# Kernel optimization log

Hardware: AMD Instinct MI355X
Metric: run time of the kernel (lower is better)

The kernel has to match this reference:

```python
import jax, jax.numpy as jnp
import numpy as np

B, N, D, H, L, R = 2, 2048, 1024, 16, 3, 2
HID = int(D * 2.67)
NASH_ITERS, SINK_ITERS = 3, 10
EPS = 1e-6


def _rmsnorm(x, w):
    return x * w * jax.lax.rsqrt(jnp.mean(x * x, axis=-1, keepdims=True) + EPS)


def _sinkhorn(logits):
    # Sinkhorn-Knopp projection of exp(logits) to a doubly-stochastic matrix
    M = jnp.exp(logits)
    for _ in range(SINK_ITERS):
        M = M / jnp.sum(M, axis=1, keepdims=True)
        M = M / jnp.sum(M, axis=0, keepdims=True)
    return M


def _swiglu(x, wg, wu, wd):
    return (jax.nn.silu(x @ wg) * (x @ wu)) @ wd


def _attention(xl, wq, wk, Wv):
    # causal multi-head attention at one scale; V projection (Wv) is shared across scales
    b, n, d = xl.shape
    dh = d // H
    q = (xl @ wq).reshape(b, n, H, dh)
    k = (xl @ wk).reshape(b, n, H, dh)
    v = (xl @ Wv).reshape(b, n, H, dh)
    scores = jnp.einsum('bqhd,bkhd->bhqk', q, k) / jnp.asarray(float(np.sqrt(dh)), xl.dtype)
    mask = jnp.tril(jnp.ones((n, n), bool))
    scores = jnp.where(mask, scores, jnp.asarray(-1e9, xl.dtype))
    p = jax.nn.softmax(scores, axis=-1)
    return jnp.einsum('bhqk,bkhd->bqhd', p, v).reshape(b, n, d)


def _forward(x, norm_attn_w, norm_ffn_w, W_dec, Wq, Wk, Wv, Wo, agg_logits,
             w_gate, w_up, w_down, mhc_attn_logits, mhc_ffn_logits):
    residual = x
    xn = _rmsnorm(x, norm_attn_w)
    # 1) hierarchical decomposition: avg-pool by R each level, per-scale projection
    scales = []
    cur = xn
    for l in range(L):
        scales.append(cur @ W_dec[l])
        if l < L - 1:
            b, n, d = cur.shape
            cur = cur.reshape(b, n // R, R, d).mean(axis=2)
    # 2) multiscale causal attention with shared V; upsample back to N and project
    outs = []
    for l in range(L):
        o = _attention(scales[l], Wq[l], Wk[l], Wv)
        o = jnp.repeat(o, R ** l, axis=1)  # [B, N, D]
        outs.append(o @ Wo)
    Y = jnp.stack(outs, axis=0)  # [L, B, N, D]
    # 3) Nash aggregation: best-response iterations on scale weights
    w = jax.nn.softmax(agg_logits)
    for _ in range(NASH_ITERS):
        y_bar = jnp.einsum('l,lbnd->bnd', w, Y)
        u = -jnp.mean((Y - y_bar[None]) ** 2, axis=(1, 2, 3))  # [L] payoffs
        w = jax.nn.softmax(agg_logits + u)
    attn_out = jnp.einsum('l,lbnd->bnd', w, Y)
    aux_loss = jnp.sum(w * jnp.log(w * L + 1e-9))  # KL(w || uniform)
    # 4) mHC residual mixing (attention branch): doubly-stochastic convex mix
    P = _sinkhorn(mhc_attn_logits)
    x = P[0, 0] * residual + P[0, 1] * attn_out
    # 5) SwiGLU FFN + mHC residual (FFN branch)
    residual = x
    xn = _rmsnorm(x, norm_ffn_w)
    ffn_out = _swiglu(xn, w_gate, w_up, w_down)
    P2 = _sinkhorn(mhc_ffn_logits)
    x = P2[0, 0] * residual + P2[0, 1] * ffn_out
    return x, aux_loss


def setup_inputs() -> dict:
    key = jax.random.key(0)
    ks = jax.random.split(key, 16)
    init = 0.02
    s = lambda i, shape: jax.random.normal(ks[i], shape, jnp.float32) * init
    return {
        'x': jax.random.normal(ks[0], (B, N, D), jnp.float32),
        'norm_attn_w': jnp.ones((D,), jnp.float32),
        'norm_ffn_w': jnp.ones((D,), jnp.float32),
        'W_dec': s(1, (L, D, D)),
        'Wq': s(2, (L, D, D)),
        'Wk': s(3, (L, D, D)),
        'Wv': s(4, (D, D)),
        'Wo': s(5, (D, D)),
        'agg_logits': jnp.zeros((L,), jnp.float32),
        'w_gate': s(6, (D, HID)),
        'w_up': s(7, (D, HID)),
        'w_down': s(8, (HID, D)),
        'mhc_attn_logits': jnp.zeros((2, 2), jnp.float32),
        'mhc_ffn_logits': jnp.zeros((2, 2), jnp.float32),
    }


def reference(x, norm_attn_w, norm_ffn_w, W_dec, Wq, Wk, Wv, Wo, agg_logits,
              w_gate, w_up, w_down, mhc_attn_logits, mhc_ffn_logits):
    return _forward(x, norm_attn_w, norm_ffn_w, W_dec, Wq, Wk, Wv, Wo, agg_logits,
                    w_gate, w_up, w_down, mhc_attn_logits, mhc_ffn_logits)
```

## Files before the change

kernel.cpp:

```cpp
#include <hip/hip_runtime.h>
#include <stdint.h>


#define B_   2
#define N_   2048
#define D_   1024
#define H_   16
#define DH_  64
#define HID_ 2734
#define HIDP 2816
#define CNT  (B_*N_*D_)
#define LOG2E 1.4426950408889634f

typedef unsigned short u16;
typedef __attribute__((ext_vector_type(8))) short short8;
typedef __attribute__((ext_vector_type(4))) float f32x4;
typedef __attribute__((ext_vector_type(4))) uint16_t u16x4;

__device__ __forceinline__ u16 f2bf(float f) {
  uint32_t u = __builtin_bit_cast(uint32_t, f);
  u += 0x7fffu + ((u >> 16) & 1u);
  return (u16)(u >> 16);
}
__device__ __forceinline__ float bf2f(u16 h) {
  uint32_t u = ((uint32_t)h) << 16;
  return __builtin_bit_cast(float, u);
}
__device__ __forceinline__ uint32_t pkbf(float a, float b) {
  return (uint32_t)f2bf(a) | ((uint32_t)f2bf(b) << 16);
}
__device__ __forceinline__ void gload_lds16(const void* g, void* l) {
  __builtin_amdgcn_global_load_lds(
      (const __attribute__((address_space(1))) uint32_t*)g,
      (__attribute__((address_space(3))) uint32_t*)l, 16, 0, 0);
}

__global__ __launch_bounds__(256) void wprep_k(const float* __restrict__ Wdec, const float* __restrict__ Wq,
                                               const float* __restrict__ Wk, const float* __restrict__ Wv,
                                               const float* __restrict__ Wo, const float* __restrict__ Wg,
                                               const float* __restrict__ Wu, const float* __restrict__ Wdn,
                                               u16* __restrict__ A_wp, u16* __restrict__ WdecB,
                                               u16* __restrict__ WoT, u16* __restrict__ BTgu,
                                               u16* __restrict__ WdnT, float* __restrict__ SCb) {
  const int bid = blockIdx.x;
  if (bid >= 18688) {
    if (bid == 18688 && threadIdx.x < 64) SCb[threadIdx.x] = 0.f;
    int i = (bid - 18688)*1024 + threadIdx.x*4;
    float4 v = *(const float4*)(Wdec + i);
    u16x4 o; o[0]=f2bf(v.x); o[1]=f2bf(v.y); o[2]=f2bf(v.z); o[3]=f2bf(v.w);
    *(u16x4*)(WdecB + i) = o;
    return;
  }
  const float* src; u16* dst; int K, N, KP; float scale; int imode; int bx, by;
  if (bid < 9216) {
    int j = bid >> 10, t = bid & 1023; bx = t & 31; by = t >> 5;
    int l = j / 3, which = j - l*3;
    src = which==0 ? Wq + (size_t)l*1048576 : which==1 ? Wk + (size_t)l*1048576 : Wv;
    dst = A_wp + (size_t)(l*3072 + which*1024)*1024;
    K = 1024; N = 1024; KP = 1024; scale = (which==0) ? 0.125f*LOG2E : 1.f; imode = 0;
  } else if (bid < 10240) {
    int t = bid - 9216; bx = t & 31; by = t >> 5;
    src = Wo; dst = WoT; K=1024; N=1024; KP=1024; scale=1.f; imode=0;
  } else if (bid < 13056) {
    int t = bid - 10240; bx = t % 88; by = t / 88;
    src = Wg; dst = BTgu; K=1024; N=HID_; KP=1024; scale=1.f; imode=1;
  } else if (bid < 15872) {
    int t = bid - 13056; bx = t % 88; by = t / 88;
    src = Wu; dst = BTgu; K=1024; N=HID_; KP=1024; scale=1.f; imode=2;
  } else {
    int t = bid - 15872; bx = t & 31; by = t >> 5;
    src = Wdn; dst = WdnT; K=HID_; N=1024; KP=HIDP; scale=1.f; imode=0;
  }
  __shared__ float tt[32][33];
  const int tx = threadIdx.x & 31, ty = threadIdx.x >> 5;
  const int nb = bx*32, kb = by*32;
  #pragma unroll
  for (int i = 0; i < 4; i++) {
    int k = kb + ty + i*8, n = nb + tx;
    tt[ty + i*8][tx] = (k < K && n < N) ? src[(size_t)k * N + n] * scale : 0.f;
  }
  __syncthreads();
  #pragma unroll
  for (int i = 0; i < 4; i++) {
    int n = nb + ty + i*8, k = kb + tx;
    int r;
    if (imode == 0) r = n;
    else if (imode == 1) r = ((n>>4)<<5) + (n&15);
    else r = ((n>>4)<<5) + 16 + (n&15);
    dst[(size_t)r * KP + k] = f2bf(tt[tx][ty + i*8]);
  }
}

__global__ __launch_bounds__(256) void rmsA_k(const float* __restrict__ x, const float* __restrict__ w,
                                              u16* __restrict__ xn, u16* __restrict__ xp1) {
  const int j = blockIdx.x;
  const float* xr0 = x + (size_t)(2*j) * D_;
  const float* xr1 = xr0 + D_;
  float a0[4], a1[4], wv[4];
  float ss0 = 0.f, ss1 = 0.f;
  #pragma unroll
  for (int i = 0; i < 4; i++) {
    int c = threadIdx.x + i*256;
    a0[i] = xr0[c]; a1[i] = xr1[c]; wv[i] = w[c];
    ss0 += a0[i]*a0[i]; ss1 += a1[i]*a1[i];
  }
  #pragma unroll
  for (int o = 1; o < 64; o <<= 1) { ss0 += __shfl_xor(ss0, o); ss1 += __shfl_xor(ss1, o); }
  __shared__ float r0[4], r1[4];
  if ((threadIdx.x & 63) == 0) { r0[threadIdx.x >> 6] = ss0; r1[threadIdx.x >> 6] = ss1; }
  __syncthreads();
  float sc0 = rsqrtf((r0[0]+r0[1]+r0[2]+r0[3]) * (1.f/D_) + 1e-6f);
  float sc1 = rsqrtf((r1[0]+r1[1]+r1[2]+r1[3]) * (1.f/D_) + 1e-6f);
  #pragma unroll
  for (int i = 0; i < 4; i++) {
    int c = threadIdx.x + i*256;
    float xa = a0[i]*wv[i]*sc0, xb = a1[i]*wv[i]*sc1;
    xn[(size_t)(2*j)*D_ + c]     = f2bf(xa);
    xn[(size_t)(2*j)*D_ + D_ + c] = f2bf(xb);
    xp1[(size_t)j*D_ + c] = f2bf(0.5f*(xa + xb));
  }
}

__global__ __launch_bounds__(256) void pool_k(const u16* __restrict__ in, u16* __restrict__ out, int lg) {
  const int No = 1 << lg;
  const int total4 = B_ * No * 256;
  for (int i = blockIdx.x*256 + threadIdx.x; i < total4; i += gridDim.x*256) {
    int d4 = i & 255; int j = (i >> 8) & (No - 1); int b = i >> (8 + lg);
    size_t src = ((size_t)(b*2*No + 2*j) << 10) + d4*4;
    u16x4 a = *(const u16x4*)(in + src);
    u16x4 c = *(const u16x4*)(in + src + 1024);
    u16x4 o;
    #pragma unroll
    for (int t = 0; t < 4; t++) o[t] = f2bf(0.5f * (bf2f(a[t]) + bf2f(c[t])));
    *(u16x4*)(out + (size_t)i*4) = o;
  }
}

template<int MT, int MODE>
__global__ __launch_bounds__(256) void gemm_t(const u16* __restrict__ A, const u16* __restrict__ BT,
                                              void* __restrict__ Cv, const float* __restrict__ X1,
                                              const float* __restrict__ SCp,
                                              int N, int K, int t1, int t2, unsigned int bt_stride) {
  __shared__ __align__(16) u16 As[MT*32*32];
  __shared__ __align__(16) u16 Bs[128*32];
  const int tid = threadIdx.x;
  const int lane = tid & 63, wid = tid >> 6;
  const int quad = lane >> 4, c16 = lane & 15;
  const int y = blockIdx.y;
  const int m0 = y * (MT*32), n0 = blockIdx.x * 128;
  const int wm = wid >> 1, wn = wid & 1;
  const int level = (y >= t2) ? 2 : ((y >= t1) ? 1 : 0);
  BT += (size_t)level * bt_stride;

  f32x4 acc[MT][4];
  #pragma unroll
  for (int i = 0; i < MT; i++)
    #pragma unroll
    for (int j = 0; j < 4; j++) acc[i][j] = f32x4{0.f,0.f,0.f,0.f};

  const int srow = lane >> 2;
  const int schunk = lane & 3;
  for (int k0 = 0; k0 < K; k0 += 32) {
    #pragma unroll
    for (int t = 0; t < MT/2; t++) {
      int idx = wid*(MT/2) + t;
      int row = idx*16 + srow;
      int g = (schunk ^ ((row >> 1) & 3)) * 8;
      gload_lds16(A + (size_t)(m0+row)*K + k0 + g, As + idx*512);
    }
    #pragma unroll
    for (int t = 0; t < 2; t++) {
      int idx = wid*2 + t;
      int row = idx*16 + srow;
      int g = (schunk ^ ((row >> 1) & 3)) * 8;
      gload_lds16(BT + (size_t)(n0+row)*K + k0 + g, Bs + idx*512);
    }
    __syncthreads();
    short8 af[MT], bfr[4];
    #pragma unroll
    for (int mt = 0; mt < MT; mt++) {
      int ar = wm*(MT*16) + mt*16 + c16;
      af[mt]  = *(const short8*)(As + ar*32 + (quad ^ ((ar>>1)&3))*8);
    }
    #pragma unroll
    for (int nt = 0; nt < 4; nt++) {
      int br = wn*64 + nt*16 + c16;
      bfr[nt] = *(const short8*)(Bs + br*32 + (quad ^ ((br>>1)&3))*8);
    }
    #pragma unroll
    for (int mt = 0; mt < MT; mt++)
      #pragma unroll
      for (int nt = 0; nt < 4; nt++)
        acc[mt][nt] = __builtin_amdgcn_mfma_f32_16x16x32_bf16(af[mt], bfr[nt], acc[mt][nt], 0, 0, 0);
    __syncthreads();
  }
  if (MODE == 1) {
    u16* C = (u16*)Cv;
    #pragma unroll
    for (int mt = 0; mt < MT; mt++)
      #pragma unroll
      for (int nt = 0; nt < 4; nt++)
        #pragma unroll
        for (int r = 0; r < 4; r++) {
          int row = m0 + wm*(MT*16) + mt*16 + quad*4 + r;
          int col = n0 + wn*64 + nt*16 + c16;
          C[(size_t)row * N + col] = f2bf(acc[mt][nt][r]);
        }
  } else if (MODE == 2) {
    float* C = (float*)Cv;
    const float q0 = SCp[11], q1 = SCp[12];
    #pragma unroll
    for (int mt = 0; mt < MT; mt++)
      #pragma unroll
      for (int nt = 0; nt < 4; nt++)
        #pragma unroll
        for (int r = 0; r < 4; r++) {
          int row = m0 + wm*(MT*16) + mt*16 + quad*4 + r;
          int col = n0 + wn*64 + nt*16 + c16;
          size_t o = (size_t)row * N + col;
          C[o] = q0 * X1[o] + q1 * acc[mt][nt][r];
        }
  } else {
    u16* Hc = (u16*)Cv;
    const int hbase = (n0 >> 1) + wn*32;
    #pragma unroll
    for (int mt = 0; mt < MT; mt++)
      #pragma unroll
      for (int r = 0; r < 4; r++) {
        int row = m0 + wm*(MT*16) + mt*16 + quad*4 + r;
        #pragma unroll
        for (int pr = 0; pr < 2; pr++) {
          float g = acc[mt][2*pr][r], u = acc[mt][2*pr+1][r];
          float h = g / (1.f + __expf(-g)) * u;
          Hc[(size_t)row * HIDP + hbase + pr*16 + c16] = f2bf(h);
        }
      }
  }
}

__global__ __launch_bounds__(256) void vtrans_k(const u16* __restrict__ QKV, u16* __restrict__ VTa) {
  __shared__ u16 t[32][33];
  const int bid = blockIdx.x;
  int level, tt2;
  if (bid < 4096)      { level = 0; tt2 = bid; }
  else if (bid < 6144) { level = 1; tt2 = bid - 4096; }
  else                 { level = 2; tt2 = bid - 6144; }
  const int Nl = 2048 >> level;
  const int ntiles = Nl >> 5;
  const int b = tt2 / (ntiles*32);
  const int rem = tt2 - b*(ntiles*32);
  const int c0 = (rem / ntiles) * 32;
  const int n0 = (rem - (rem / ntiles)*ntiles) * 32;
  const int rowbase = (level==0) ? 0 : (level==1) ? 4096 : 6144;
  const size_t vtoff = (level==0) ? 0 : (level==1) ? 4194304 : 6291456;
  const u16* in = QKV + (size_t)rowbase*3072 + 2048;
  u16* out = VTa + vtoff;
  const int tx = threadIdx.x & 31, ty = threadIdx.x >> 5;
  #pragma unroll
  for (int i = 0; i < 4; i++)
    t[ty + i*8][tx] = in[(size_t)(b*Nl + n0 + ty + i*8)*3072 + c0 + tx];
  __syncthreads();
  #pragma unroll
  for (int i = 0; i < 4; i++)
    out[(size_t)(b*1024 + c0 + ty + i*8)*Nl + n0 + tx] = t[tx][ty + i*8];
}

__global__ __launch_bounds__(256) void flash_k(const u16* __restrict__ QKVg,
                                               const u16* __restrict__ VTg,
                                               u16* __restrict__ Og) {
  __shared__ __align__(16) u16 Kt[2][64*64];
  __shared__ __align__(16) u16 Vt[2][64*64];
  __shared__ __align__(16) u16 Ps[4][32*68];
  const int tid = threadIdx.x, lane = tid & 63, wid = tid >> 6;
  const int quad = lane >> 4, c16 = lane & 15;
  const int id = blockIdx.x;
  int qt, bh, Nl, rowbase; size_t vtoff;
  if (id < 512)      { qt = 15 - (id >> 5);            bh = id & 31;  Nl = 2048; rowbase = 0;    vtoff = 0; }
  else if (id < 768) { int t2 = id - 512; qt = 7 - (t2 >> 5); bh = t2 & 31; Nl = 1024; rowbase = 4096; vtoff = 4194304; }
  else               { int t2 = id - 768; qt = 3 - (t2 >> 5); bh = t2 & 31; Nl = 512;  rowbase = 6144; vtoff = 6291456; }
  const int b = bh >> 4, h = bh & 15;
  const u16* QK = QKVg + ((size_t)(rowbase + b*Nl)) * 3072 + h*64;
  u16* Ow = Og + ((size_t)(rowbase + b*Nl)) * 1024 + h*64;
  const u16* VT = VTg + vtoff + ((size_t)b*1024 + h*64) * (size_t)Nl;

  const int q0r = qt*128 + wid*32;
  short8 bq[2][2];
  #pragma unroll
  for (int qh = 0; qh < 2; qh++) {
    const u16* qp = QK + (size_t)(q0r + qh*16 + c16)*3072 + quad*8;
    bq[qh][0] = *(const short8*)qp;
    bq[qh][1] = *(const short8*)(qp + 32);
  }
  const int si0 = wid*2, si1 = si0 + 1;
  const int sr0 = si0*8 + (lane>>3), sr1 = si1*8 + (lane>>3);
  const int sg  = ((lane&7) ^ (lane>>3)) * 8;
  const u16* Ks0 = QK + 1024 + (size_t)sr0*3072 + sg;
  const u16* Ks1 = QK + 1024 + (size_t)sr1*3072 + sg;
  const u16* Vs0 = VT + (size_t)sr0*Nl + sg;
  const u16* Vs1 = VT + (size_t)sr1*Nl + sg;

  f32x4 oacc[2][4];
  f32x4 lacc[2];
  #pragma unroll
  for (int qh = 0; qh < 2; qh++) {
    lacc[qh] = f32x4{0.f,0.f,0.f,0.f};
    #pragma unroll
    for (int nt = 0; nt < 4; nt++) oacc[qh][nt] = f32x4{0.f,0.f,0.f,0.f};
  }

  auto stage = [&](int kt, int p) {
    const size_t ko = (size_t)kt * 64;
    gload_lds16(Ks0 + ko*3072, &Kt[p][si0*512]);
    gload_lds16(Ks1 + ko*3072, &Kt[p][si1*512]);
    gload_lds16(Vs0 + ko,      &Vt[p][si0*512]);
    gload_lds16(Vs1 + ko,      &Vt[p][si1*512]);
  };
  const int kmax_w = 2*qt + (wid >> 1);
  const int ktot   = 2*qt + 2;
  stage(0, 0);

  for (int kt = 0; kt < ktot; kt++) {
    const int p = kt & 1;
    __syncthreads();
    if (kt + 1 < ktot) stage(kt+1, p^1);
    if (kt > kmax_w) continue;

    f32x4 st[2][4];
    #pragma unroll
    for (int nt = 0; nt < 4; nt++) {
      int key = nt*16 + c16, x = key & 7;
      short8 a0 = *(const short8*)(&Kt[p][key*64 + ((quad    ) ^ x)*8]);
      short8 a1 = *(const short8*)(&Kt[p][key*64 + ((quad + 4) ^ x)*8]);
      #pragma unroll
      for (int qh = 0; qh < 2; qh++) {
        f32x4 s = f32x4{0.f,0.f,0.f,0.f};
        s = __builtin_amdgcn_mfma_f32_16x16x32_bf16(a0, bq[qh][0], s, 0, 0, 0);
        s = __builtin_amdgcn_mfma_f32_16x16x32_bf16(a1, bq[qh][1], s, 0, 0, 0);
        st[qh][nt] = s;
      }
    }
    if (kt >= 2*qt) {
      const int kb = kt*64;
      #pragma unroll
      for (int qh = 0; qh < 2; qh++) {
        const int qr = q0r + qh*16 + c16;
        #pragma unroll
        for (int nt = 0; nt < 4; nt++) {
          #pragma unroll
          for (int r = 0; r < 4; r++) {
            float e = __builtin_amdgcn_exp2f(st[qh][nt][r]);
            st[qh][nt][r] = (kb + nt*16 + quad*4 + r <= qr) ? e : 0.f;
          }
          lacc[qh] += st[qh][nt];
        }
      }
    } else {
      #pragma unroll
      for (int qh = 0; qh < 2; qh++)
        #pragma unroll
        for (int nt = 0; nt < 4; nt++) {
          #pragma unroll
          for (int r = 0; r < 4; r++) st[qh][nt][r] = __builtin_amdgcn_exp2f(st[qh][nt][r]);
          lacc[qh] += st[qh][nt];
        }
    }
    #pragma unroll
    for (int qh = 0; qh < 2; qh++) {
      const int prow = qh*16 + c16;
      #pragma unroll
      for (int nt = 0; nt < 4; nt++) {
        uint2 pk;
        pk.x = pkbf(st[qh][nt][0], st[qh][nt][1]);
        pk.y = pkbf(st[qh][nt][2], st[qh][nt][3]);
        *(uint2*)(&Ps[wid][prow*68 + nt*16 + quad*4]) = pk;
      }
    }
    short8 bp[2][2];
    #pragma unroll
    for (int qh = 0; qh < 2; qh++) {
      bp[qh][0] = *(const short8*)(&Ps[wid][(qh*16 + c16)*68 +      quad*8]);
      bp[qh][1] = *(const short8*)(&Ps[wid][(qh*16 + c16)*68 + 32 + quad*8]);
    }
    #pragma unroll
    for (int nt = 0; nt < 4; nt++) {
      int dh = nt*16 + c16, x = dh & 7;
      short8 a0 = *(const short8*)(&Vt[p][dh*64 + ((quad    ) ^ x)*8]);
      short8 a1 = *(const short8*)(&Vt[p][dh*64 + ((quad + 4) ^ x)*8]);
      #pragma unroll
      for (int qh = 0; qh < 2; qh++) {
        oacc[qh][nt] = __builtin_amdgcn_mfma_f32_16x16x32_bf16(a0, bp[qh][0], oacc[qh][nt], 0, 0, 0);
        oacc[qh][nt] = __builtin_amdgcn_mfma_f32_16x16x32_bf16(a1, bp[qh][1], oacc[qh][nt], 0, 0, 0);
      }
    }
  }
  #pragma unroll
  for (int qh = 0; qh < 2; qh++) {
    float ls = lacc[qh][0] + lacc[qh][1] + lacc[qh][2] + lacc[qh][3];
    ls += __shfl_xor(ls, 16);
    ls += __shfl_xor(ls, 32);
    const float rl = 1.f / ls;
    #pragma unroll
    for (int nt = 0; nt < 4; nt++) {
      uint2 o;
      o.x = pkbf(oacc[qh][nt][0]*rl, oacc[qh][nt][1]*rl);
      o.y = pkbf(oacc[qh][nt][2]*rl, oacc[qh][nt][3]*rl);
      *(uint2*)(Ow + (size_t)(q0r + qh*16 + c16)*1024 + nt*16 + quad*4) = o;
    }
  }
}

__global__ __launch_bounds__(256) void gram_k(const u16* __restrict__ Y0, const u16* __restrict__ Y1,
                                              const u16* __restrict__ Y2, float* __restrict__ G) {
  float a[6] = {0,0,0,0,0,0};
  const int total4 = CNT/4;
  for (int i = blockIdx.x*256 + threadIdx.x; i < total4; i += gridDim.x*256) {
    int d4 = i & 255; int n = (i >> 8) & (N_-1); int b = i >> 19;
    u16x4 y0v = *(const u16x4*)(Y0 + (size_t)i*4);
    u16x4 y1v = *(const u16x4*)(Y1 + (((size_t)(b*1024 + (n>>1))) << 10) + d4*4);
    u16x4 y2v = *(const u16x4*)(Y2 + (((size_t)(b*512  + (n>>2))) << 10) + d4*4);
    #pragma unroll
    for (int t = 0; t < 4; t++) {
      float y0 = bf2f(y0v[t]), y1 = bf2f(y1v[t]), y2 = bf2f(y2v[t]);
      a[0] += y0*y0; a[1] += y0*y1; a[2] += y0*y2;
      a[3] += y1*y1; a[4] += y1*y2; a[5] += y2*y2;
    }
  }
  __shared__ float red[4][6];
  const int lane = threadIdx.x & 63, wid = threadIdx.x >> 6;
  #pragma unroll
  for (int t = 0; t < 6; t++) {
    float v = a[t];
    v += __shfl_xor(v, 1);  v += __shfl_xor(v, 2);  v += __shfl_xor(v, 4);
    v += __shfl_xor(v, 8);  v += __shfl_xor(v, 16); v += __shfl_xor(v, 32);
    a[t] = v;
  }
  if (lane == 0)
    #pragma unroll
    for (int t = 0; t < 6; t++) red[wid][t] = a[t];
  __syncthreads();
  if (threadIdx.x < 6)
    atomicAdd(&G[threadIdx.x], red[0][threadIdx.x] + red[1][threadIdx.x] +
                               red[2][threadIdx.x] + red[3][threadIdx.x]);
}

__global__ void head_k(float* SC, const float* __restrict__ agg, const float* __restrict__ mA,
                       const float* __restrict__ mF, float* __restrict__ aux_out) {
  if (threadIdx.x != 0 || blockIdx.x != 0) return;
  float G[6];
  for (int t = 0; t < 6; t++) G[t] = SC[t];
  const int gi[3][3] = {{0,1,2},{1,3,4},{2,4,5}};
  float a[3] = {agg[0], agg[1], agg[2]};
  float w[3];
  {
    float m = fmaxf(a[0], fmaxf(a[1], a[2])); float s = 0.f;
    for (int l = 0; l < 3; l++) { w[l] = expf(a[l]-m); s += w[l]; }
    for (int l = 0; l < 3; l++) w[l] /= s;
  }
  const float inv = 1.f / (float)CNT;
  for (int it = 0; it < 3; it++) {
    float q = 0.f;
    for (int l = 0; l < 3; l++) for (int m2 = 0; m2 < 3; m2++) q += w[l]*w[m2]*G[gi[l][m2]];
    float z[3];
    for (int l = 0; l < 3; l++) {
      float dot = w[0]*G[gi[l][0]] + w[1]*G[gi[l][1]] + w[2]*G[gi[l][2]];
      z[l] = a[l] - (G[gi[l][l]] - 2.f*dot + q) * inv;
    }
    float m = fmaxf(z[0], fmaxf(z[1], z[2])); float s = 0.f;
    for (int l = 0; l < 3; l++) { w[l] = expf(z[l]-m); s += w[l]; }
    for (int l = 0; l < 3; l++) w[l] /= s;
  }
  SC[6] = w[0]; SC[7] = w[1]; SC[8] = w[2];
  aux_out[0] = w[0]*logf(w[0]*3.f + 1e-9f) + w[1]*logf(w[1]*3.f + 1e-9f) + w[2]*logf(w[2]*3.f + 1e-9f);
  for (int which = 0; which < 2; which++) {
    const float* Lg = which ? mF : mA;
    float M0 = expf(Lg[0]), M1 = expf(Lg[1]), M2 = expf(Lg[2]), M3 = expf(Lg[3]);
    for (int i2 = 0; i2 < 10; i2++) {
      float r0 = M0+M1, r1 = M2+M3; M0 /= r0; M1 /= r0; M2 /= r1; M3 /= r1;
      float c0 = M0+M2, c1 = M1+M3; M0 /= c0; M2 /= c0; M1 /= c1; M3 /= c1;
    }
    SC[9 + which*2] = M0; SC[10 + which*2] = M1;
  }
}

__global__ __launch_bounds__(256) void mixrms_k(const float* __restrict__ x, const u16* __restrict__ Y0,
                                                const u16* __restrict__ Y1, const u16* __restrict__ Y2,
                                                const float* __restrict__ SC, const float* __restrict__ w2,
                                                float* __restrict__ x1, u16* __restrict__ xn2) {
  const float w0 = SC[6], w1 = SC[7], ww2 = SC[8], p0 = SC[9], p1 = SC[10];
  const int i = blockIdx.x;
  const int b = i >> 11, n = i & 2047;
  const float* xr = x + (size_t)i * D_;
  const u16* y0 = Y0 + (size_t)i * D_;
  const u16* y1 = Y1 + (size_t)(b*1024 + (n>>1)) * D_;
  const u16* y2 = Y2 + (size_t)(b*512  + (n>>2)) * D_;
  float xv[4], wv[4];
  float ss = 0.f;
  #pragma unroll
  for (int t = 0; t < 4; t++) {
    int c = threadIdx.x + t*256;
    float v = p0*xr[c] + p1*(w0*bf2f(y0[c]) + w1*bf2f(y1[c]) + ww2*bf2f(y2[c]));
    xv[t] = v; wv[t] = w2[c]; ss += v*v;
    x1[(size_t)i*D_ + c] = v;
  }
  #pragma unroll
  for (int o = 1; o < 64; o <<= 1) ss += __shfl_xor(ss, o);
  __shared__ float red[4];
  if ((threadIdx.x & 63) == 0) red[threadIdx.x >> 6] = ss;
  __syncthreads();
  float sc = rsqrtf((red[0]+red[1]+red[2]+red[3]) * (1.f/D_) + 1e-6f);
  #pragma unroll
  for (int t = 0; t < 4; t++) {
    int c = threadIdx.x + t*256;
    xn2[(size_t)i*D_ + c] = f2bf(xv[t]*wv[t]*sc);
  }
}

extern "C" void kernel_launch(void* const* d_in, const int* in_sizes, int n_in,
                              void* d_out, int out_size, void* d_ws, size_t ws_size,
                              hipStream_t stream) {
  (void)in_sizes; (void)n_in; (void)out_size; (void)ws_size;
  const float* x    = (const float*)d_in[0];
  const float* nw1  = (const float*)d_in[1];
  const float* nw2  = (const float*)d_in[2];
  const float* Wdec = (const float*)d_in[3];
  const float* Wq   = (const float*)d_in[4];
  const float* Wk   = (const float*)d_in[5];
  const float* Wv   = (const float*)d_in[6];
  const float* Wo   = (const float*)d_in[7];
  const float* agg  = (const float*)d_in[8];
  const float* Wg   = (const float*)d_in[9];
  const float* Wu   = (const float*)d_in[10];
  const float* Wdn  = (const float*)d_in[11];
  const float* mA   = (const float*)d_in[12];
  const float* mF   = (const float*)d_in[13];
  float* out = (float*)d_out;

  char* ws = (char*)d_ws;
  size_t off = 0;
  auto take = [&](size_t b) { size_t r = off; off += (b + 255) & ~(size_t)255; return r; };

  u16* A_wp  = (u16*)(ws + take((size_t)9216*1024*2));
  u16* WdecB = (u16*)(ws + take((size_t)3*1024*1024*2));
  u16* Wqkv  = (u16*)(ws + take((size_t)9216*1024*2));
  u16* BTgu  = (u16*)(ws + take((size_t)5632*1024*2));
  u16* WdnT  = (u16*)(ws + take((size_t)HIDP*1024*2));
  u16* WoT   = (u16*)(ws + take((size_t)1024*1024*2));
  u16* xn_all = (u16*)(ws + take((size_t)7168*1024*2));
  float* x1  = (float*)(ws + take((size_t)CNT*4));
  float* SCb = (float*)(ws + take(256));
  char*  big = ws + take(88080384);
  u16*   QKV   = (u16*)big;
  u16*   VTa   = (u16*)(big + 44040192);
  u16*   Ob    = (u16*)(big + 58720256);
  u16*   YC    = (u16*)(big + 73400320);
  u16*   hbuf  = (u16*)big;

  dim3 blk(256);
  const int BIG = 1 << 30;

  wprep_k<<<21760, blk, 0, stream>>>(Wdec, Wq, Wk, Wv, Wo, Wg, Wu, Wdn,
                                     A_wp, WdecB, WoT, BTgu, WdnT, SCb);
  gemm_t<4,1><<<dim3(8, 72), blk, 0, stream>>>(A_wp, WdecB, Wqkv, nullptr, nullptr,
                                               1024, 1024, 24, 48, 1024u*1024u);
  rmsA_k<<<2048, blk, 0, stream>>>(x, nw1, xn_all, xn_all + (size_t)4096*1024);
  pool_k<<<512, blk, 0, stream>>>(xn_all + (size_t)4096*1024, xn_all + (size_t)6144*1024, 9);
  gemm_t<4,1><<<dim3(24, 56), blk, 0, stream>>>(xn_all, Wqkv, QKV, nullptr, nullptr,
                                                3072, 1024, 32, 48, 3072u*1024u);
  vtrans_k<<<7168, blk, 0, stream>>>(QKV, VTa);
  flash_k<<<896, blk, 0, stream>>>(QKV, VTa, Ob);
  gemm_t<2,1><<<dim3(8, 112), blk, 0, stream>>>(Ob, WoT, YC, nullptr, nullptr,
                                                1024, 1024, BIG, BIG, 0u);
  u16* YC1 = YC + (size_t)4096*1024;
  u16* YC2 = YC + (size_t)6144*1024;
  gram_k<<<1024, blk, 0, stream>>>(YC, YC1, YC2, SCb);
  head_k<<<1, 64, 0, stream>>>(SCb, agg, mA, mF, out + CNT);
  mixrms_k<<<4096, blk, 0, stream>>>(x, YC, YC1, YC2, SCb, nw2, x1, xn_all);
  gemm_t<4,3><<<dim3(44, 32), blk, 0, stream>>>(xn_all, BTgu, hbuf, nullptr, nullptr,
                                                5632, 1024, BIG, BIG, 0u);
  gemm_t<2,2><<<dim3(8, 64), blk, 0, stream>>>(hbuf, WdnT, out, x1, SCb,
                                               1024, HIDP, BIG, BIG, 0u);
}
```

Baseline: 505.0 us.

## Compute V transposed directly via GEMM, fuse pooling and gram/head kernels

Splits the QKV projection so the main GEMM produces only Q and K. A new GEMM kernel computes V^T directly from the weights and normalized inputs, which removes the separate transpose pass and the V write/read round trip. RMSNorm now processes four rows per block and emits both pooled levels, so the separate pool kernel is gone. The gram reduction and the scalar head kernel are merged using a last-block atomic counter, saving one launch. The risks are an untuned V GEMM with strided stores and reliance on the counter slot in the scratch buffer being zero-initialised.

After: 591.6 us. 1.17x slower.

```diff
diff --git a/kernel.cpp b/kernel.cpp
--- a/kernel.cpp
+++ b/kernel.cpp
@@ -92,47 +92,46 @@
 }
 
 __global__ __launch_bounds__(256) void rmsA_k(const float* __restrict__ x, const float* __restrict__ w,
-                                              u16* __restrict__ xn, u16* __restrict__ xp1) {
+                                              u16* __restrict__ xn, u16* __restrict__ xp1,
+                                              u16* __restrict__ xp2) {
   const int j = blockIdx.x;
-  const float* xr0 = x + (size_t)(2*j) * D_;
-  const float* xr1 = xr0 + D_;
-  float a0[4], a1[4], wv[4];
-  float ss0 = 0.f, ss1 = 0.f;
+  const float* xr = x + (size_t)(4*j) * D_;
+  float a[4][4], wv[4];
+  float ss[4] = {0.f, 0.f, 0.f, 0.f};
   #pragma unroll
   for (int i = 0; i < 4; i++) {
     int c = threadIdx.x + i*256;
-    a0[i] = xr0[c]; a1[i] = xr1[c]; wv[i] = w[c];
-    ss0 += a0[i]*a0[i]; ss1 += a1[i]*a1[i];
-  }
-  #pragma unroll
-  for (int o = 1; o < 64; o <<= 1) { ss0 += __shfl_xor(ss0, o); ss1 += __shfl_xor(ss1, o); }
-  __shared__ float r0[4], r1[4];
-  if ((threadIdx.x & 63) == 0) { r0[threadIdx.x >> 6] = ss0; r1[threadIdx.x >> 6] = ss1; }
+    wv[i] = w[c];
+    #pragma unroll
+    for (int r = 0; r < 4; r++) { float v = xr[(size_t)r*D_ + c]; a[r][i] = v; ss[r] += v*v; }
+  }
+  #pragma unroll
+  for (int o = 1; o < 64; o <<= 1) {
+    #pragma unroll
+    for (int r = 0; r < 4; r++) ss[r] += __shfl_xor(ss[r], o);
+  }
+  __shared__ float red[4][4];
+  if ((threadIdx.x & 63) == 0) {
+    #pragma unroll
+    for (int r = 0; r < 4; r++) red[threadIdx.x >> 6][r] = ss[r];
+  }
   __syncthreads();
-  float sc0 = rsqrtf((r0[0]+r0[1]+r0[2]+r0[3]) * (1.f/D_) + 1e-6f);
-  float sc1 = rsqrtf((r1[0]+r1[1]+r1[2]+r1[3]) * (1.f/D_) + 1e-6f);
+  float sc[4];
+  #pragma unroll
+  for (int r = 0; r < 4; r++)
+    sc[r] = rsqrtf((red[0][r]+red[1][r]+red[2][r]+red[3][r]) * (1.f/D_) + 1e-6f);
   #pragma unroll
   for (int i = 0; i < 4; i++) {
     int c = threadIdx.x + i*256;
-    float xa = a0[i]*wv[i]*sc0, xb = a1[i]*wv[i]*sc1;
-    xn[(size_t)(2*j)*D_ + c]     = f2bf(xa);
-    xn[(size_t)(2*j)*D_ + D_ + c] = f2bf(xb);
-    xp1[(size_t)j*D_ + c] = f2bf(0.5f*(xa + xb));
-  }
-}
-
-__global__ __launch_bounds__(256) void pool_k(const u16* __restrict__ in, u16* __restrict__ out, int lg) {
-  const int No = 1 << lg;
-  const int total4 = B_ * No * 256;
-  for (int i = blockIdx.x*256 + threadIdx.x; i < total4; i += gridDim.x*256) {
-    int d4 = i & 255; int j = (i >> 8) & (No - 1); int b = i >> (8 + lg);
-    size_t src = ((size_t)(b*2*No + 2*j) << 10) + d4*4;
-    u16x4 a = *(const u16x4*)(in + src);
-    u16x4 c = *(const u16x4*)(in + src + 1024);
-    u16x4 o;
-    #pragma unroll
-    for (int t = 0; t < 4; t++) o[t] = f2bf(0.5f * (bf2f(a[t]) + bf2f(c[t])));
-    *(u16x4*)(out + (size_t)i*4) = o;
+    float v0 = a[0][i]*wv[i]*sc[0], v1 = a[1][i]*wv[i]*sc[1];
+    float v2 = a[2][i]*wv[i]*sc[2], v3 = a[3][i]*wv[i]*sc[3];
+    xn[(size_t)(4*j  )*D_ + c] = f2bf(v0);
+    xn[(size_t)(4*j+1)*D_ + c] = f2bf(v1);
+    xn[(size_t)(4*j+2)*D_ + c] = f2bf(v2);
+    xn[(size_t)(4*j+3)*D_ + c] = f2bf(v3);
+    xp1[(size_t)(2*j  )*D_ + c] = f2bf(0.5f*(v0+v1));
+    xp1[(size_t)(2*j+1)*D_ + c] = f2bf(0.5f*(v2+v3));
+    xp2[(size_t)j*D_ + c] = f2bf(0.25f*(v0+v1+v2+v3));
   }
 }
 
@@ -238,31 +237,72 @@
   }
 }
 
-__global__ __launch_bounds__(256) void vtrans_k(const u16* __restrict__ QKV, u16* __restrict__ VTa) {
-  __shared__ u16 t[32][33];
-  const int bid = blockIdx.x;
-  int level, tt2;
-  if (bid < 4096)      { level = 0; tt2 = bid; }
-  else if (bid < 6144) { level = 1; tt2 = bid - 4096; }
-  else                 { level = 2; tt2 = bid - 6144; }
+__global__ __launch_bounds__(256) void vgemm_k(const u16* __restrict__ Wqkv, const u16* __restrict__ xn_all,
+                                               u16* __restrict__ VTa) {
+  const int z = blockIdx.z, level = z >> 1, b = z & 1;
   const int Nl = 2048 >> level;
-  const int ntiles = Nl >> 5;
-  const int b = tt2 / (ntiles*32);
-  const int rem = tt2 - b*(ntiles*32);
-  const int c0 = (rem / ntiles) * 32;
-  const int n0 = (rem - (rem / ntiles)*ntiles) * 32;
+  if (blockIdx.x * 128 >= Nl) return;
   const int rowbase = (level==0) ? 0 : (level==1) ? 4096 : 6144;
   const size_t vtoff = (level==0) ? 0 : (level==1) ? 4194304 : 6291456;
-  const u16* in = QKV + (size_t)rowbase*3072 + 2048;
-  u16* out = VTa + vtoff;
-  const int tx = threadIdx.x & 31, ty = threadIdx.x >> 5;
+  const u16* A  = Wqkv + (size_t)level*3072*1024 + (size_t)2048*1024;
+  const u16* BT = xn_all + (size_t)(rowbase + b*Nl) * 1024;
+  u16* C = VTa + vtoff + (size_t)b*1024*Nl;
+  const int K = 1024;
+
+  __shared__ __align__(16) u16 As[128*32];
+  __shared__ __align__(16) u16 Bs[128*32];
+  const int tid = threadIdx.x;
+  const int lane = tid & 63, wid = tid >> 6;
+  const int quad = lane >> 4, c16 = lane & 15;
+  const int m0 = blockIdx.y * 128, n0 = blockIdx.x * 128;
+  const int wm = wid >> 1, wn = wid & 1;
+
+  f32x4 acc[4][4];
   #pragma unroll
   for (int i = 0; i < 4; i++)
-    t[ty + i*8][tx] = in[(size_t)(b*Nl + n0 + ty + i*8)*3072 + c0 + tx];
-  __syncthreads();
-  #pragma unroll
-  for (int i = 0; i < 4; i++)
-    out[(size_t)(b*1024 + c0 + ty + i*8)*Nl + n0 + tx] = t[tx][ty + i*8];
+    #pragma unroll
+    for (int j = 0; j < 4; j++) acc[i][j] = f32x4{0.f,0.f,0.f,0.f};
+
+  const int srow = lane >> 2;
+  const int schunk = lane & 3;
+  for (int k0 = 0; k0 < K; k0 += 32) {
+    #pragma unroll
+    for (int t = 0; t < 2; t++) {
+      int idx = wid*2 + t;
+      int row = idx*16 + srow;
+      int g = (schunk ^ ((row >> 1) & 3)) * 8;
+      gload_lds16(A  + (size_t)(m0+row)*K + k0 + g, As + idx*512);
+      gload_lds16(BT + (size_t)(n0+row)*K + k0 + g, Bs + idx*512);
+    }
+    __syncthreads();
+    short8 af[4], bfr[4];
+    #pragma unroll
+    for (int mt = 0; mt < 4; mt++) {
+      int ar = wm*64 + mt*16 + c16;
+      af[mt]  = *(const short8*)(As + ar*32 + (quad ^ ((ar>>1)&3))*8);
+    }
+    #pragma unroll
+    for (int nt = 0; nt < 4; nt++) {
+      int br = wn*64 + nt*16 + c16;
+      bfr[nt] = *(const short8*)(Bs + br*32 + (quad ^ ((br>>1)&3))*8);
+    }
+    #pragma unroll
+    for (int mt = 0; mt < 4; mt++)
+      #pragma unroll
+      for (int nt = 0; nt < 4; nt++)
+        acc[mt][nt] = __builtin_amdgcn_mfma_f32_16x16x32_bf16(af[mt], bfr[nt], acc[mt][nt], 0, 0, 0);
+    __syncthreads();
+  }
+  #pragma unroll
+  for (int mt = 0; mt < 4; mt++)
+    #pragma unroll
+    for (int nt = 0; nt < 4; nt++)
+      #pragma unroll
+      for (int r = 0; r < 4; r++) {
+        int row = m0 + wm*64 + mt*16 + quad*4 + r;
+        int col = n0 + wn*64 + nt*16 + c16;
+        C[(size_t)row * Nl + col] = f2bf(acc[mt][nt][r]);
+      }
 }
 
 __global__ __launch_bounds__(256) void flash_k(const u16* __restrict__ QKVg,
@@ -279,7 +319,7 @@
   else if (id < 768) { int t2 = id - 512; qt = 7 - (t2 >> 5); bh = t2 & 31; Nl = 1024; rowbase = 4096; vtoff = 4194304; }
   else               { int t2 = id - 768; qt = 3 - (t2 >> 5); bh = t2 & 31; Nl = 512;  rowbase = 6144; vtoff = 6291456; }
   const int b = bh >> 4, h = bh & 15;
-  const u16* QK = QKVg + ((size_t)(rowbase + b*Nl)) * 3072 + h*64;
+  const u16* QK = QKVg + ((size_t)(rowbase + b*Nl)) * 2048 + h*64;
   u16* Ow = Og + ((size_t)(rowbase + b*Nl)) * 1024 + h*64;
   const u16* VT = VTg + vtoff + ((size_t)b*1024 + h*64) * (size_t)Nl;
 
@@ -287,15 +327,15 @@
   short8 bq[2][2];
   #pragma unroll
   for (int qh = 0; qh < 2; qh++) {
-    const u16* qp = QK + (size_t)(q0r + qh*16 + c16)*3072 + quad*8;
+    const u16* qp = QK + (size_t)(q0r + qh*16 + c16)*2048 + quad*8;
     bq[qh][0] = *(const short8*)qp;
     bq[qh][1] = *(const short8*)(qp + 32);
   }
   const int si0 = wid*2, si1 = si0 + 1;
   const int sr0 = si0*8 + (lane>>3), sr1 = si1*8 + (lane>>3);
   const int sg  = ((lane&7) ^ (lane>>3)) * 8;
-  const u16* Ks0 = QK + 1024 + (size_t)sr0*3072 + sg;
-  const u16* Ks1 = QK + 1024 + (size_t)sr1*3072 + sg;
+  const u16* Ks0 = QK + 1024 + (size_t)sr0*2048 + sg;
+  const u16* Ks1 = QK + 1024 + (size_t)sr1*2048 + sg;
   const u16* Vs0 = VT + (size_t)sr0*Nl + sg;
   const u16* Vs1 = VT + (size_t)sr1*Nl + sg;
 
@@ -310,8 +350,8 @@
 
   auto stage = [&](int kt, int p) {
     const size_t ko = (size_t)kt * 64;
-    gload_lds16(Ks0 + ko*3072, &Kt[p][si0*512]);
-    gload_lds16(Ks1 + ko*3072, &Kt[p][si1*512]);
+    gload_lds16(Ks0 + ko*2048, &Kt[p][si0*512]);
+    gload_lds16(Ks1 + ko*2048, &Kt[p][si1*512]);
     gload_lds16(Vs0 + ko,      &Vt[p][si0*512]);
     gload_lds16(Vs1 + ko,      &Vt[p][si1*512]);
   };
@@ -409,8 +449,10 @@
   }
 }
 
-__global__ __launch_bounds__(256) void gram_k(const u16* __restrict__ Y0, const u16* __restrict__ Y1,
-                                              const u16* __restrict__ Y2, float* __restrict__ G) {
+__global__ __launch_bounds__(256) void gramhead_k(const u16* __restrict__ Y0, const u16* __restrict__ Y1,
+                                                  const u16* __restrict__ Y2, float* __restrict__ SC,
+                                                  const float* __restrict__ agg, const float* __restrict__ mA,
+                                                  const float* __restrict__ mF, float* __restrict__ aux_out) {
   float a[6] = {0,0,0,0,0,0};
   const int total4 = CNT/4;
   for (int i = blockIdx.x*256 + threadIdx.x; i < total4; i += gridDim.x*256) {
@@ -438,22 +480,23 @@
     #pragma unroll
     for (int t = 0; t < 6; t++) red[wid][t] = a[t];
   __syncthreads();
-  if (threadIdx.x < 6)
-    atomicAdd(&G[threadIdx.x], red[0][threadIdx.x] + red[1][threadIdx.x] +
-                               red[2][threadIdx.x] + red[3][threadIdx.x]);
-}
-
-__global__ void head_k(float* SC, const float* __restrict__ agg, const float* __restrict__ mA,
-                       const float* __restrict__ mF, float* __restrict__ aux_out) {
-  if (threadIdx.x != 0 || blockIdx.x != 0) return;
+  if (threadIdx.x != 0) return;
+  #pragma unroll
+  for (int t = 0; t < 6; t++)
+    atomicAdd(&SC[t], red[0][t] + red[1][t] + red[2][t] + red[3][t]);
+  __threadfence();
+  unsigned int* cnt = (unsigned int*)(SC + 32);
+  unsigned int old = atomicAdd(cnt, 1u);
+  if (old != gridDim.x - 1) return;
+  __threadfence();
   float G[6];
-  for (int t = 0; t < 6; t++) G[t] = SC[t];
+  for (int t = 0; t < 6; t++) G[t] = atomicAdd(&SC[t], 0.f);
   const int gi[3][3] = {{0,1,2},{1,3,4},{2,4,5}};
-  float a[3] = {agg[0], agg[1], agg[2]};
+  float ag[3] = {agg[0], agg[1], agg[2]};
   float w[3];
   {
-    float m = fmaxf(a[0], fmaxf(a[1], a[2])); float s = 0.f;
-    for (int l = 0; l < 3; l++) { w[l] = expf(a[l]-m); s += w[l]; }
+    float m = fmaxf(ag[0], fmaxf(ag[1], ag[2])); float s = 0.f;
+    for (int l = 0; l < 3; l++) { w[l] = expf(ag[l]-m); s += w[l]; }
     for (int l = 0; l < 3; l++) w[l] /= s;
   }
   const float inv = 1.f / (float)CNT;
@@ -463,7 +506,7 @@
     float z[3];
     for (int l = 0; l < 3; l++) {
       float dot = w[0]*G[gi[l][0]] + w[1]*G[gi[l][1]] + w[2]*G[gi[l][2]];
-      z[l] = a[l] - (G[gi[l][l]] - 2.f*dot + q) * inv;
+      z[l] = ag[l] - (G[gi[l][l]] - 2.f*dot + q) * inv;
     }
     float m = fmaxf(z[0], fmaxf(z[1], z[2])); float s = 0.f;
     for (int l = 0; l < 3; l++) { w[l] = expf(z[l]-m); s += w[l]; }
@@ -550,9 +593,9 @@
   float* SCb = (float*)(ws + take(256));
   char*  big = ws + take(88080384);
   u16*   QKV   = (u16*)big;
-  u16*   VTa   = (u16*)(big + 44040192);
-  u16*   Ob    = (u16*)(big + 58720256);
-  u16*   YC    = (u16*)(big + 73400320);
+  u16*   VTa   = (u16*)(big + 29360128);
+  u16*   Ob    = (u16*)(big + 44040192);
+  u16*   YC    = (u16*)(big + 58720256);
   u16*   hbuf  = (u16*)big;
 
   dim3 blk(256);
@@ -562,18 +605,17 @@
                                      A_wp, WdecB, WoT, BTgu, WdnT, SCb);
   gemm_t<4,1><<<dim3(8, 72), blk, 0, stream>>>(A_wp, WdecB, Wqkv, nullptr, nullptr,
                                                1024, 1024, 24, 48, 1024u*1024u);
-  rmsA_k<<<2048, blk, 0, stream>>>(x, nw1, xn_all, xn_all + (size_t)4096*1024);
-  pool_k<<<512, blk, 0, stream>>>(xn_all + (size_t)4096*1024, xn_all + (size_t)6144*1024, 9);
-  gemm_t<4,1><<<dim3(24, 56), blk, 0, stream>>>(xn_all, Wqkv, QKV, nullptr, nullptr,
-                                                3072, 1024, 32, 48, 3072u*1024u);
-  vtrans_k<<<7168, blk, 0, stream>>>(QKV, VTa);
+  rmsA_k<<<1024, blk, 0, stream>>>(x, nw1, xn_all,
+                                   xn_all + (size_t)4096*1024, xn_all + (size_t)6144*1024);
+  gemm_t<4,1><<<dim3(16, 56), blk, 0, stream>>>(xn_all, Wqkv, QKV, nullptr, nullptr,
+                                                2048, 1024, 32, 48, 3072u*1024u);
+  vgemm_k<<<dim3(16, 8, 6), blk, 0, stream>>>(Wqkv, xn_all, VTa);
   flash_k<<<896, blk, 0, stream>>>(QKV, VTa, Ob);
   gemm_t<2,1><<<dim3(8, 112), blk, 0, stream>>>(Ob, WoT, YC, nullptr, nullptr,
                                                 1024, 1024, BIG, BIG, 0u);
   u16* YC1 = YC + (size_t)4096*1024;
   u16* YC2 = YC + (size_t)6144*1024;
-  gram_k<<<1024, blk, 0, stream>>>(YC, YC1, YC2, SCb);
-  head_k<<<1, 64, 0, stream>>>(SCb, agg, mA, mF, out + CNT);
+  gramhead_k<<<1024, blk, 0, stream>>>(YC, YC1, YC2, SCb, agg, mA, mF, out + CNT);
   mixrms_k<<<4096, blk, 0, stream>>>(x, YC, YC1, YC2, SCb, nw2, x1, xn_all);
   gemm_t<4,3><<<dim3(44, 32), blk, 0, stream>>>(xn_all, BTgu, hbuf, nullptr, nullptr,
                                                 5632, 1024, BIG, BIG, 0u);
```
